# Kernel optimization log

Measured on AMD Instinct MI355X. Metric: run time of the kernel, lower is better.

## Reference

```python
import jax, jax.numpy as jnp
import numpy as np

DIM = 1024
HEADS = 16
HEAD_DIM = DIM // HEADS


def _rope(x, cos, sin):
    # x: [B, H, L, Dh]; cos/sin: [L, Dh//2]
    x1 = x[..., ::2]
    x2 = x[..., 1::2]
    xr1 = x1 * cos - x2 * sin
    xr2 = x1 * sin + x2 * cos
    # interleave back: stack on last dim then flatten -> [..., Dh]
    return jnp.stack([xr1, xr2], axis=-1).reshape(x.shape)


def setup_inputs() -> dict:
    key = jax.random.key(0)
    k1, k2, k3 = jax.random.split(key, 3)
    B, L = 4, 2048
    x = jax.random.normal(k1, (B, L, DIM), dtype=jnp.float32)
    # weights stored [in, out]; scaled like kaiming-ish init
    w_qkv = jax.random.normal(k2, (DIM, 3 * DIM), dtype=jnp.float32) / np.sqrt(DIM)
    w_proj = jax.random.normal(k3, (DIM, DIM), dtype=jnp.float32) / np.sqrt(DIM)
    return {"x": x, "w_qkv": w_qkv, "w_proj": w_proj}


def reference(x, w_qkv, w_proj):
    B, L, D = x.shape
    H, Dh = HEADS, HEAD_DIM

    qkv = x @ w_qkv                      # [B, L, 3D]
    q, k, v = jnp.split(qkv, 3, axis=-1)

    def reshape(t):
        return t.reshape(B, L, H, Dh).transpose(0, 2, 1, 3)  # [B, H, L, Dh]

    q, k, v = reshape(q), reshape(k), reshape(v)

    # RoPE tables
    theta = 10000.0
    inv_freq = 1.0 / theta ** (jnp.arange(0, Dh, 2, dtype=jnp.float32) / Dh)
    t = jnp.arange(L, dtype=jnp.float32)
    freqs = jnp.einsum('l,d->ld', t, inv_freq)   # [L, Dh//2]
    cos, sin = jnp.cos(freqs), jnp.sin(freqs)

    q = _rope(q, cos, sin)
    k = _rope(k, cos, sin)

    scale = 1.0 / np.sqrt(Dh).astype(np.float32)
    attn = jnp.einsum('bhqd,bhkd->bhqk', q, k) * scale   # [B, H, L, L]
    attn = jax.nn.softmax(attn, axis=-1)
    out = jnp.einsum('bhqk,bhkd->bhqd', attn, v)          # [B, H, L, Dh]
    out = out.transpose(0, 2, 1, 3).reshape(B, L, D)
    return out @ w_proj
```

## Files before the change

kernel.cpp:

```cpp
#include <hip/hip_runtime.h>

#define L_SEQ   2048
#define D_MODEL 1024
#define N_QKV   3072

typedef __attribute__((ext_vector_type(8)))  short short8;
typedef __attribute__((ext_vector_type(4)))  float f32x4;
typedef __attribute__((ext_vector_type(16))) float f32x16;

__device__ __forceinline__ unsigned short f2bf(float f){
    unsigned int u = __float_as_uint(f);
    u += 0x7fffu + ((u >> 16) & 1u);
    return (unsigned short)(u >> 16);
}

__device__ __forceinline__ void gload16(const void* g, void* l){
    __builtin_amdgcn_global_load_lds(
        (const __attribute__((address_space(1))) unsigned int*)g,
        (__attribute__((address_space(3))) unsigned int*)l, 16, 0, 0);
}

__device__ __forceinline__ unsigned int cvtpk_bf16(float lo, float hi){
    unsigned int r;
    asm volatile("v_cvt_pk_bf16_f32 %0, %1, %2" : "=v"(r) : "v"(lo), "v"(hi));
    return r;
}

__global__ void rope_table_kernel(float* __restrict__ cost, float* __restrict__ sint){
    int idx = blockIdx.x * blockDim.x + threadIdx.x;
    if (idx >= L_SEQ * 32) return;
    int l = idx >> 5;
    int i = idx & 31;
    double e = (double)(2 * i) / 64.0;
    float invf = (float)pow(10000.0, -e);
    float f = (float)l * invf;
    cost[idx] = cosf(f);
    sint[idx] = sinf(f);
}

__global__ __launch_bounds__(256) void cvt_bf16_kernel(
    const float* __restrict__ in, unsigned short* __restrict__ out)
{
    int i = (blockIdx.x * 256 + threadIdx.x) * 4;
    float4 v = *(const float4*)(in + i);
    ushort4 o;
    o.x = f2bf(v.x); o.y = f2bf(v.y); o.z = f2bf(v.z); o.w = f2bf(v.w);
    *(ushort4*)(out + i) = o;
}

__global__ __launch_bounds__(256) void transpose_bf16_kernel(
    const float* __restrict__ W, unsigned short* __restrict__ WT, int K, int N)
{
    __shared__ float T[64][65];
    const int k0 = blockIdx.y * 64, n0 = blockIdx.x * 64;
    const int r  = threadIdx.x >> 4;
    const int c4 = (threadIdx.x & 15) * 4;
    #pragma unroll
    for (int i = 0; i < 4; ++i){
        int row = r + i * 16;
        float4 v = *(const float4*)&W[(size_t)(k0 + row) * N + n0 + c4];
        T[row][c4 + 0] = v.x; T[row][c4 + 1] = v.y;
        T[row][c4 + 2] = v.z; T[row][c4 + 3] = v.w;
    }
    __syncthreads();
    #pragma unroll
    for (int i = 0; i < 4; ++i){
        int nl = r + i * 16;
        ushort4 o;
        o.x = f2bf(T[c4 + 0][nl]); o.y = f2bf(T[c4 + 1][nl]);
        o.z = f2bf(T[c4 + 2][nl]); o.w = f2bf(T[c4 + 3][nl]);
        *(ushort4*)&WT[(size_t)(n0 + nl) * K + k0 + c4] = o;
    }
}

__global__ __launch_bounds__(256, 3) void qkv_mfma_kernel(
    const unsigned short* __restrict__ A, const unsigned short* __restrict__ BT,
    const float* __restrict__ cost, const float* __restrict__ sint,
    unsigned short* __restrict__ qb, unsigned short* __restrict__ kb,
    unsigned short* __restrict__ vtb)
{
    __shared__ __align__(16) unsigned char smem[34816];
    unsigned short* Al = (unsigned short*)smem;
    unsigned short* Bl = Al + 8192;
    unsigned short* T  = (unsigned short*)smem;

    const int tid  = threadIdx.x;
    const int lane = tid & 63;
    const int w    = tid >> 6;
    const int wm   = w & 1, wn = w >> 1;
    const int l15  = lane & 15, l4 = lane >> 4;
    const int m0   = blockIdx.y * 128;
    const int n0   = blockIdx.x * 128;

    const int srow = tid >> 3;
    const int scol = ((tid & 7) * 8) ^ ((srow & 7) * 8);
    const int ksw  = (l15 & 7) * 8;

    f32x4 acc[4][4];
    #pragma unroll
    for (int i = 0; i < 4; ++i)
        #pragma unroll
        for (int j = 0; j < 4; ++j)
            acc[i][j] = (f32x4){0.f, 0.f, 0.f, 0.f};

    for (int k0 = 0; k0 < 1024; k0 += 64){
        #pragma unroll
        for (int c = 0; c < 4; ++c){
            gload16(&A [(size_t)(m0 + c * 32 + srow) * 1024 + k0 + scol],
                    &Al[c * 2048 + w * 512]);
            gload16(&BT[(size_t)(n0 + c * 32 + srow) * 1024 + k0 + scol],
                    &Bl[c * 2048 + w * 512]);
        }
        __syncthreads();
        #pragma unroll
        for (int kc = 0; kc < 2; ++kc){
            short8 a[4], b[4];
            #pragma unroll
            for (int mi = 0; mi < 4; ++mi)
                a[mi] = *(const short8*)&Al[(wm * 64 + mi * 16 + l15) * 64 + ((kc * 32 + l4 * 8) ^ ksw)];
            #pragma unroll
            for (int ni = 0; ni < 4; ++ni)
                b[ni] = *(const short8*)&Bl[(wn * 64 + ni * 16 + l15) * 64 + ((kc * 32 + l4 * 8) ^ ksw)];
            #pragma unroll
            for (int mi = 0; mi < 4; ++mi)
                #pragma unroll
                for (int ni = 0; ni < 4; ++ni)
                    acc[mi][ni] = __builtin_amdgcn_mfma_f32_16x16x32_bf16(a[mi], b[ni], acc[mi][ni], 0, 0, 0);
        }
        __syncthreads();
    }

    const int which = n0 >> 10;
    #pragma unroll
    for (int ni = 0; ni < 4; ++ni){
        const int c  = wn * 64 + ni * 16 + l15;
        const int d  = (n0 + c) & 63;
        const int fi = d >> 1;
        const float sgn = (d & 1) ? 1.0f : -1.0f;
        #pragma unroll
        for (int mi = 0; mi < 4; ++mi){
            const int row0 = wm * 64 + mi * 16 + l4 * 4;
            if (which == 2){
                ushort4 pk;
                pk.x = f2bf(acc[mi][ni][0]); pk.y = f2bf(acc[mi][ni][1]);
                pk.z = f2bf(acc[mi][ni][2]); pk.w = f2bf(acc[mi][ni][3]);
                *(ushort4*)&T[c * 136 + row0] = pk;
            } else {
                #pragma unroll
                for (int r = 0; r < 4; ++r){
                    int row = row0 + r;
                    int gl  = (m0 + row) & 2047;
                    float val = acc[mi][ni][r];
                    float cs = cost[gl * 32 + fi];
                    float sn = sint[gl * 32 + fi];
                    float partner = __shfl_xor(val, 1);
                    float outv = val * cs + sgn * partner * sn;
                    if (which == 0) outv *= 0.125f;
                    T[row * 136 + c] = f2bf(outv);
                }
            }
        }
    }
    __syncthreads();

    const int bidx = m0 >> 11;
    if (which == 2){
        #pragma unroll
        for (int it = 0; it < 8; ++it){
            int chunk = it * 256 + tid;
            int crow  = chunk >> 4;
            int lch   = chunk & 15;
            short8 v = *(const short8*)&T[crow * 136 + lch * 8];
            int colg = n0 + crow;
            int hh   = (colg & 1023) >> 6;
            int d    = colg & 63;
            int l0   = (m0 & 2047) + lch * 8;
            *(short8*)&vtb[(((size_t)(bidx * 16 + hh)) * 64 + d) * 2048 + l0] = v;
        }
    } else {
        unsigned short* dstb = (which == 0) ? qb : kb;
        #pragma unroll
        for (int it = 0; it < 8; ++it){
            int chunk = it * 256 + tid;
            int row   = chunk >> 4;
            int ch    = chunk & 15;
            short8 v = *(const short8*)&T[row * 136 + ch * 8];
            int gl   = (m0 & 2047) + row;
            int colg = n0 + ch * 8;
            int hh   = (colg & 1023) >> 6;
            int d0   = colg & 63;
            *(short8*)&dstb[(((size_t)(bidx * 16 + hh)) * 2048 + gl) * 64 + d0] = v;
        }
    }
}

__global__ __launch_bounds__(256, 3) void proj_mfma_kernel(
    const unsigned short* __restrict__ A, const unsigned short* __restrict__ BT,
    float* __restrict__ C)
{
    __shared__ __align__(16) unsigned short Al[128 * 64];
    __shared__ __align__(16) unsigned short Bl[128 * 64];

    const int tid  = threadIdx.x;
    const int lane = tid & 63;
    const int w    = tid >> 6;
    const int wm   = w & 1, wn = w >> 1;
    const int l15  = lane & 15, l4 = lane >> 4;
    const int m0   = blockIdx.y * 128;
    const int n0   = blockIdx.x * 128;

    const int srow = tid >> 3;
    const int scol = ((tid & 7) * 8) ^ ((srow & 7) * 8);
    const int ksw  = (l15 & 7) * 8;

    f32x4 acc[4][4];
    #pragma unroll
    for (int i = 0; i < 4; ++i)
        #pragma unroll
        for (int j = 0; j < 4; ++j)
            acc[i][j] = (f32x4){0.f, 0.f, 0.f, 0.f};

    for (int k0 = 0; k0 < 1024; k0 += 64){
        #pragma unroll
        for (int c = 0; c < 4; ++c){
            gload16(&A [(size_t)(m0 + c * 32 + srow) * 1024 + k0 + scol],
                    &Al[c * 2048 + w * 512]);
            gload16(&BT[(size_t)(n0 + c * 32 + srow) * 1024 + k0 + scol],
                    &Bl[c * 2048 + w * 512]);
        }
        __syncthreads();
        #pragma unroll
        for (int kc = 0; kc < 2; ++kc){
            short8 a[4], b[4];
            #pragma unroll
            for (int mi = 0; mi < 4; ++mi)
                a[mi] = *(const short8*)&Al[(wm * 64 + mi * 16 + l15) * 64 + ((kc * 32 + l4 * 8) ^ ksw)];
            #pragma unroll
            for (int ni = 0; ni < 4; ++ni)
                b[ni] = *(const short8*)&Bl[(wn * 64 + ni * 16 + l15) * 64 + ((kc * 32 + l4 * 8) ^ ksw)];
            #pragma unroll
            for (int mi = 0; mi < 4; ++mi)
                #pragma unroll
                for (int ni = 0; ni < 4; ++ni)
                    acc[mi][ni] = __builtin_amdgcn_mfma_f32_16x16x32_bf16(a[mi], b[ni], acc[mi][ni], 0, 0, 0);
        }
        __syncthreads();
    }

    #pragma unroll
    for (int mi = 0; mi < 4; ++mi)
        #pragma unroll
        for (int r = 0; r < 4; ++r){
            int row = m0 + wm * 64 + mi * 16 + l4 * 4 + r;
            #pragma unroll
            for (int ni = 0; ni < 4; ++ni){
                int colc = n0 + wn * 64 + ni * 16 + l15;
                C[(size_t)row * 1024 + colc] = acc[mi][ni][r];
            }
        }
}

__global__ __launch_bounds__(512, 4) void attn_mfma32_kernel(
    const unsigned short* __restrict__ qb,
    const unsigned short* __restrict__ kb,
    const unsigned short* __restrict__ vtb,
    unsigned short* __restrict__ ctx)
{
    __shared__ __align__(16) unsigned char lds[49152];

    const int tid  = threadIdx.x;
    const int lane = tid & 63;
    const int w    = tid >> 6;
    const int l31  = lane & 31;
    const int hi   = lane >> 5;
    const int blk = blockIdx.x;
    const int swz = ((blk & 7) << 6) | (blk >> 3);
    const int bh  = swz >> 3;
    const int qt  = swz & 7;
    const int b   = bh >> 4, h = bh & 15;

    const unsigned short* Kg  = kb  + (size_t)bh * 2048 * 64;
    const unsigned short* VTg = vtb + (size_t)bh * 64 * 2048;
    const int q0 = qt * 256 + w * 32;
    const unsigned short* Qg = qb + ((size_t)bh * 2048 + q0) * 64;

    short8 qf[4];
    #pragma unroll
    for (int kbd = 0; kbd < 4; ++kbd)
        qf[kbd] = *(const short8*)(Qg + l31 * 64 + hi * 8 + kbd * 16);

    f32x16 o0, o1;
    f32x4  lsv = (f32x4){0.f, 0.f, 0.f, 0.f};
    #pragma unroll
    for (int r = 0; r < 16; ++r){ o0[r] = 0.f; o1[r] = 0.f; }

    const unsigned short* ksrc = Kg + ((size_t)((w >> 2) * 32 + l31)) * 64 + hi * 8 + (w & 3) * 16;
    const unsigned short* vsrc = VTg + ((size_t)((w >> 2) * 32 + l31)) * 2048 + hi * 8 + (w & 3) * 16;

    auto STAGE = [&](int t, int buf){
        unsigned char* base = lds + buf * 16384 + w * 1024;
        gload16(ksrc + (size_t)t * 4096, base);
        gload16(vsrc + (size_t)t * 64, base + 8192);
    };

    STAGE(0, 0);
    STAGE(1, 1);

    int bufc = 0;
    for (int t = 0; t < 32; ++t){
        if (t < 31){
            asm volatile("s_waitcnt vmcnt(2)" ::: "memory");
        } else {
            asm volatile("s_waitcnt vmcnt(0)" ::: "memory");
        }
        __builtin_amdgcn_s_barrier();
        if (t < 30) STAGE(t + 2, (bufc == 0) ? 2 : bufc - 1);

        unsigned char* Kl = lds + bufc * 16384;
        unsigned char* Vl = Kl + 8192;

        short8 pa[4];
        #pragma unroll
        for (int g = 0; g < 2; ++g){
            f32x16 acc;
            #pragma unroll
            for (int r = 0; r < 16; ++r) acc[r] = -16.0f;
            short8 kf0 = *(const short8*)(Kl + (g * 4 + 0) * 1024 + lane * 16);
            short8 kf1 = *(const short8*)(Kl + (g * 4 + 1) * 1024 + lane * 16);
            short8 kf2 = *(const short8*)(Kl + (g * 4 + 2) * 1024 + lane * 16);
            short8 kf3 = *(const short8*)(Kl + (g * 4 + 3) * 1024 + lane * 16);
            __builtin_amdgcn_s_setprio(1);
            acc = __builtin_amdgcn_mfma_f32_32x32x16_bf16(kf0, qf[0], acc, 0, 0, 0);
            acc = __builtin_amdgcn_mfma_f32_32x32x16_bf16(kf1, qf[1], acc, 0, 0, 0);
            acc = __builtin_amdgcn_mfma_f32_32x32x16_bf16(kf2, qf[2], acc, 0, 0, 0);
            acc = __builtin_amdgcn_mfma_f32_32x32x16_bf16(kf3, qf[3], acc, 0, 0, 0);
            __builtin_amdgcn_s_setprio(0);
            #pragma unroll
            for (int r = 0; r < 16; ++r){
                float p = __expf(acc[r]);
                acc[r] = p;
                lsv[r & 3] += p;
            }
            #pragma unroll
            for (int half = 0; half < 2; ++half){
                unsigned int w01 = cvtpk_bf16(acc[half*8+0], acc[half*8+1]);
                unsigned int w23 = cvtpk_bf16(acc[half*8+2], acc[half*8+3]);
                unsigned int w45 = cvtpk_bf16(acc[half*8+4], acc[half*8+5]);
                unsigned int w67 = cvtpk_bf16(acc[half*8+6], acc[half*8+7]);
                asm volatile("v_permlane32_swap_b32 %0, %1" : "+v"(w01), "+v"(w45));
                asm volatile("v_permlane32_swap_b32 %0, %1" : "+v"(w23), "+v"(w67));
                short8 pp;
                pp[0] = (short)(w01 & 0xffffu); pp[1] = (short)(w01 >> 16);
                pp[2] = (short)(w23 & 0xffffu); pp[3] = (short)(w23 >> 16);
                pp[4] = (short)(w45 & 0xffffu); pp[5] = (short)(w45 >> 16);
                pp[6] = (short)(w67 & 0xffffu); pp[7] = (short)(w67 >> 16);
                pa[g * 2 + half] = pp;
            }
        }

        #pragma unroll
        for (int kbv = 0; kbv < 4; ++kbv){
            short8 vf0 = *(const short8*)(Vl + (0 * 4 + kbv) * 1024 + lane * 16);
            short8 vf1 = *(const short8*)(Vl + (1 * 4 + kbv) * 1024 + lane * 16);
            __builtin_amdgcn_s_setprio(1);
            o0 = __builtin_amdgcn_mfma_f32_32x32x16_bf16(vf0, pa[kbv], o0, 0, 0, 0);
            o1 = __builtin_amdgcn_mfma_f32_32x32x16_bf16(vf1, pa[kbv], o1, 0, 0, 0);
            __builtin_amdgcn_s_setprio(0);
        }

        bufc = (bufc == 2) ? 0 : bufc + 1;
    }

    float ls = lsv[0] + lsv[1] + lsv[2] + lsv[3];
    ls += __shfl_xor(ls, 32);
    float inv = 1.0f / ls;

    size_t crow = (size_t)b * 2048 + q0 + l31;
    unsigned short* cp = ctx + crow * 1024 + h * 64;
    #pragma unroll
    for (int r = 0; r < 16; ++r){
        int d = (r & 3) + 8 * (r >> 2) + 4 * hi;
        cp[d]      = f2bf(o0[r] * inv);
        cp[d + 32] = f2bf(o1[r] * inv);
    }
}

extern "C" void kernel_launch(void* const* d_in, const int* in_sizes, int n_in,
                              void* d_out, int out_size, void* d_ws, size_t ws_size,
                              hipStream_t stream) {
    const float* x      = (const float*)d_in[0];
    const float* w_qkv  = (const float*)d_in[1];
    const float* w_proj = (const float*)d_in[2];
    float* out = (float*)d_out;

    char* ws = (char*)d_ws;
    float*          cost   = (float*)(ws);
    float*          sint   = (float*)(ws + 262144);
    unsigned short* xbf    = (unsigned short*)(ws + 524288);
    unsigned short* qb     = (unsigned short*)(ws + 17301504);
    unsigned short* kb     = (unsigned short*)(ws + 34078720);
    unsigned short* vtb    = (unsigned short*)(ws + 50855936);
    unsigned short* wqkvT  = (unsigned short*)(ws + 67633152);
    unsigned short* wprojT = (unsigned short*)(ws + 73924608);
    unsigned short* ctxbf  = xbf;

    rope_table_kernel<<<256, 256, 0, stream>>>(cost, sint);

    cvt_bf16_kernel<<<8192, 256, 0, stream>>>(x, xbf);

    dim3 gt1(48, 16);
    transpose_bf16_kernel<<<gt1, 256, 0, stream>>>(w_qkv, wqkvT, 1024, 3072);
    dim3 gt2(16, 16);
    transpose_bf16_kernel<<<gt2, 256, 0, stream>>>(w_proj, wprojT, 1024, 1024);

    dim3 g1(24, 64);
    qkv_mfma_kernel<<<g1, 256, 0, stream>>>(xbf, wqkvT, cost, sint, qb, kb, vtb);

    attn_mfma32_kernel<<<512, 512, 0, stream>>>(qb, kb, vtb, ctxbf);

    dim3 g3(8, 64);
    proj_mfma_kernel<<<g3, 256, 0, stream>>>(ctxbf, wprojT, out);
}
```

Measured before the change: 188.2 us.

## Triple-buffer K tiles with async LDS loads in QKV and proj GEMMs

Replaces the single-buffered load/sync/compute loop in the QKV and output-projection GEMMs with a 3-stage ring buffer of 32-wide K tiles. Loads for tile t+2 are issued before computing tile t, with vmcnt waits and one barrier per step instead of two. The LDS swizzle is changed to fit the 32-column tiles, and s_setprio raises wave priority around the MFMA block. LDS use grows to 48KB per block, which may reduce occupancy below the launch-bounds target.

```diff
diff --git a/kernel.cpp b/kernel.cpp
--- a/kernel.cpp
+++ b/kernel.cpp
@@ -79,10 +79,8 @@
     unsigned short* __restrict__ qb, unsigned short* __restrict__ kb,
     unsigned short* __restrict__ vtb)
 {
-    __shared__ __align__(16) unsigned char smem[34816];
-    unsigned short* Al = (unsigned short*)smem;
-    unsigned short* Bl = Al + 8192;
-    unsigned short* T  = (unsigned short*)smem;
+    __shared__ __align__(16) unsigned char smem[49152];
+    unsigned short* T = (unsigned short*)smem;
 
     const int tid  = threadIdx.x;
     const int lane = tid & 63;
@@ -92,9 +90,8 @@
     const int m0   = blockIdx.y * 128;
     const int n0   = blockIdx.x * 128;
 
-    const int srow = tid >> 3;
-    const int scol = ((tid & 7) * 8) ^ ((srow & 7) * 8);
-    const int ksw  = (l15 & 7) * 8;
+    const int srow_lo = tid >> 2;
+    const int sch     = tid & 3;
 
     f32x4 acc[4][4];
     #pragma unroll
@@ -103,32 +100,58 @@
         for (int j = 0; j < 4; ++j)
             acc[i][j] = (f32x4){0.f, 0.f, 0.f, 0.f};
 
-    for (int k0 = 0; k0 < 1024; k0 += 64){
-        #pragma unroll
-        for (int c = 0; c < 4; ++c){
-            gload16(&A [(size_t)(m0 + c * 32 + srow) * 1024 + k0 + scol],
-                    &Al[c * 2048 + w * 512]);
-            gload16(&BT[(size_t)(n0 + c * 32 + srow) * 1024 + k0 + scol],
-                    &Bl[c * 2048 + w * 512]);
-        }
-        __syncthreads();
-        #pragma unroll
-        for (int kc = 0; kc < 2; ++kc){
-            short8 a[4], b[4];
-            #pragma unroll
-            for (int mi = 0; mi < 4; ++mi)
-                a[mi] = *(const short8*)&Al[(wm * 64 + mi * 16 + l15) * 64 + ((kc * 32 + l4 * 8) ^ ksw)];
+    auto STAGE = [&](int t, int buf){
+        unsigned char* base = smem + buf * 16384;
+        const int k0 = t * 32;
+        #pragma unroll
+        for (int c = 0; c < 2; ++c){
+            int row = c * 64 + srow_lo;
+            int ssw = ((sch * 8) ^ (((row >> 1) & 3) * 8));
+            gload16(&A [(size_t)(m0 + row) * 1024 + k0 + ssw],
+                    base + c * 4096 + w * 1024);
+            gload16(&BT[(size_t)(n0 + row) * 1024 + k0 + ssw],
+                    base + 8192 + c * 4096 + w * 1024);
+        }
+    };
+
+    STAGE(0, 0);
+    STAGE(1, 1);
+
+    int bufc = 0;
+    for (int t = 0; t < 32; ++t){
+        if (t < 31){
+            asm volatile("s_waitcnt vmcnt(4)" ::: "memory");
+        } else {
+            asm volatile("s_waitcnt vmcnt(0)" ::: "memory");
+        }
+        __builtin_amdgcn_s_barrier();
+        if (t < 30) STAGE(t + 2, (bufc == 0) ? 2 : bufc - 1);
+
+        unsigned short* Al = (unsigned short*)(smem + bufc * 16384);
+        unsigned short* Bl = Al + 4096;
+
+        short8 a[4], b[4];
+        #pragma unroll
+        for (int mi = 0; mi < 4; ++mi){
+            int row = wm * 64 + mi * 16 + l15;
+            a[mi] = *(const short8*)&Al[row * 32 + ((l4 * 8) ^ (((row >> 1) & 3) * 8))];
+        }
+        #pragma unroll
+        for (int ni = 0; ni < 4; ++ni){
+            int row = wn * 64 + ni * 16 + l15;
+            b[ni] = *(const short8*)&Bl[row * 32 + ((l4 * 8) ^ (((row >> 1) & 3) * 8))];
+        }
+        __builtin_amdgcn_s_setprio(1);
+        #pragma unroll
+        for (int mi = 0; mi < 4; ++mi)
             #pragma unroll
             for (int ni = 0; ni < 4; ++ni)
-                b[ni] = *(const short8*)&Bl[(wn * 64 + ni * 16 + l15) * 64 + ((kc * 32 + l4 * 8) ^ ksw)];
-            #pragma unroll
-            for (int mi = 0; mi < 4; ++mi)
-                #pragma unroll
-                for (int ni = 0; ni < 4; ++ni)
-                    acc[mi][ni] = __builtin_amdgcn_mfma_f32_16x16x32_bf16(a[mi], b[ni], acc[mi][ni], 0, 0, 0);
-        }
-        __syncthreads();
-    }
+                acc[mi][ni] = __builtin_amdgcn_mfma_f32_16x16x32_bf16(a[mi], b[ni], acc[mi][ni], 0, 0, 0);
+        __builtin_amdgcn_s_setprio(0);
+
+        bufc = (bufc == 2) ? 0 : bufc + 1;
+    }
+    __syncthreads();
 
     const int which = n0 >> 10;
     #pragma unroll
@@ -198,8 +221,7 @@
     const unsigned short* __restrict__ A, const unsigned short* __restrict__ BT,
     float* __restrict__ C)
 {
-    __shared__ __align__(16) unsigned short Al[128 * 64];
-    __shared__ __align__(16) unsigned short Bl[128 * 64];
+    __shared__ __align__(16) unsigned char smem[49152];
 
     const int tid  = threadIdx.x;
     const int lane = tid & 63;
@@ -209,9 +231,8 @@
     const int m0   = blockIdx.y * 128;
     const int n0   = blockIdx.x * 128;
 
-    const int srow = tid >> 3;
-    const int scol = ((tid & 7) * 8) ^ ((srow & 7) * 8);
-    const int ksw  = (l15 & 7) * 8;
+    const int srow_lo = tid >> 2;
+    const int sch     = tid & 3;
 
     f32x4 acc[4][4];
     #pragma unroll
@@ -220,31 +241,56 @@
         for (int j = 0; j < 4; ++j)
             acc[i][j] = (f32x4){0.f, 0.f, 0.f, 0.f};
 
-    for (int k0 = 0; k0 < 1024; k0 += 64){
-        #pragma unroll
-        for (int c = 0; c < 4; ++c){
-            gload16(&A [(size_t)(m0 + c * 32 + srow) * 1024 + k0 + scol],
-                    &Al[c * 2048 + w * 512]);
-            gload16(&BT[(size_t)(n0 + c * 32 + srow) * 1024 + k0 + scol],
-                    &Bl[c * 2048 + w * 512]);
-        }
-        __syncthreads();
-        #pragma unroll
-        for (int kc = 0; kc < 2; ++kc){
-            short8 a[4], b[4];
-            #pragma unroll
-            for (int mi = 0; mi < 4; ++mi)
-                a[mi] = *(const short8*)&Al[(wm * 64 + mi * 16 + l15) * 64 + ((kc * 32 + l4 * 8) ^ ksw)];
+    auto STAGE = [&](int t, int buf){
+        unsigned char* base = smem + buf * 16384;
+        const int k0 = t * 32;
+        #pragma unroll
+        for (int c = 0; c < 2; ++c){
+            int row = c * 64 + srow_lo;
+            int ssw = ((sch * 8) ^ (((row >> 1) & 3) * 8));
+            gload16(&A [(size_t)(m0 + row) * 1024 + k0 + ssw],
+                    base + c * 4096 + w * 1024);
+            gload16(&BT[(size_t)(n0 + row) * 1024 + k0 + ssw],
+                    base + 8192 + c * 4096 + w * 1024);
+        }
+    };
+
+    STAGE(0, 0);
+    STAGE(1, 1);
+
+    int bufc = 0;
+    for (int t = 0; t < 32; ++t){
+        if (t < 31){
+            asm volatile("s_waitcnt vmcnt(4)" ::: "memory");
+        } else {
+            asm volatile("s_waitcnt vmcnt(0)" ::: "memory");
+        }
+        __builtin_amdgcn_s_barrier();
+        if (t < 30) STAGE(t + 2, (bufc == 0) ? 2 : bufc - 1);
+
+        unsigned short* Al = (unsigned short*)(smem + bufc * 16384);
+        unsigned short* Bl = Al + 4096;
+
+        short8 a[4], b[4];
+        #pragma unroll
+        for (int mi = 0; mi < 4; ++mi){
+            int row = wm * 64 + mi * 16 + l15;
+            a[mi] = *(const short8*)&Al[row * 32 + ((l4 * 8) ^ (((row >> 1) & 3) * 8))];
+        }
+        #pragma unroll
+        for (int ni = 0; ni < 4; ++ni){
+            int row = wn * 64 + ni * 16 + l15;
+            b[ni] = *(const short8*)&Bl[row * 32 + ((l4 * 8) ^ (((row >> 1) & 3) * 8))];
+        }
+        __builtin_amdgcn_s_setprio(1);
+        #pragma unroll
+        for (int mi = 0; mi < 4; ++mi)
             #pragma unroll
             for (int ni = 0; ni < 4; ++ni)
-                b[ni] = *(const short8*)&Bl[(wn * 64 + ni * 16 + l15) * 64 + ((kc * 32 + l4 * 8) ^ ksw)];
-            #pragma unroll
-            for (int mi = 0; mi < 4; ++mi)
-                #pragma unroll
-                for (int ni = 0; ni < 4; ++ni)
-                    acc[mi][ni] = __builtin_amdgcn_mfma_f32_16x16x32_bf16(a[mi], b[ni], acc[mi][ni], 0, 0, 0);
-        }
-        __syncthreads();
+                acc[mi][ni] = __builtin_amdgcn_mfma_f32_16x16x32_bf16(a[mi], b[ni], acc[mi][ni], 0, 0, 0);
+        __builtin_amdgcn_s_setprio(0);
+
+        bufc = (bufc == 2) ? 0 : bufc + 1;
     }
 
     #pragma unroll
```

New measurement: 201.0 us. +6.8%, slower.
